# Performance work log

Hardware: AMD Instinct MI355X
Metric: run time of the kernel (lower is better)

## Reference

```python
import jax, jax.numpy as jnp
import numpy as np

B, S, H, I, NH, E = 16, 512, 1024, 4096, 16, 8
DH = H // NH
EPS = 1e-12


def layer_norm(x, g, b):
    mu = jnp.mean(x, axis=-1, keepdims=True)
    var = jnp.mean(jnp.square(x - mu), axis=-1, keepdims=True)
    return (x - mu) * jax.lax.rsqrt(var + EPS) * g + b


def setup_inputs() -> dict:
    key = jax.random.key(0)
    ks = jax.random.split(key, 16)
    s_h = 1.0 / np.sqrt(H)
    s_i = 1.0 / np.sqrt(I)
    return {
        "hidden_states": jax.random.normal(ks[0], (B, S, H), jnp.float32),
        "Wq": jax.random.normal(ks[1], (H, H), jnp.float32) * s_h,
        "bq": jnp.zeros((H,), jnp.float32),
        "Wk": jax.random.normal(ks[2], (H, H), jnp.float32) * s_h,
        "bk": jnp.zeros((H,), jnp.float32),
        "Wv": jax.random.normal(ks[3], (H, H), jnp.float32) * s_h,
        "bv": jnp.zeros((H,), jnp.float32),
        "Wo": jax.random.normal(ks[4], (H, H), jnp.float32) * s_h,
        "bo": jnp.zeros((H,), jnp.float32),
        "ln1_g": jnp.ones((H,), jnp.float32),
        "ln1_b": jnp.zeros((H,), jnp.float32),
        "ln2_g": jnp.ones((H,), jnp.float32),
        "ln2_b": jnp.zeros((H,), jnp.float32),
        "gate_W": jax.random.normal(ks[5], (H, E), jnp.float32) * s_h,
        "W_up": jax.random.normal(ks[6], (E, H, I), jnp.float32) * s_h,
        "b_up": jnp.zeros((E, I), jnp.float32),
        "W_down": jax.random.normal(ks[7], (E, I, H), jnp.float32) * s_i,
        "b_down": jnp.zeros((E, H), jnp.float32),
    }


def reference(hidden_states, Wq, bq, Wk, bk, Wv, bv, Wo, bo,
              ln1_g, ln1_b, ln2_g, ln2_b, gate_W, W_up, b_up, W_down, b_down):
    x = hidden_states
    # --- BERT self-attention ---
    q = (x @ Wq + bq).reshape(B, S, NH, DH)
    k = (x @ Wk + bk).reshape(B, S, NH, DH)
    v = (x @ Wv + bv).reshape(B, S, NH, DH)
    scores = jnp.einsum("bqhd,bkhd->bhqk", q, k) / np.sqrt(DH)
    probs = jax.nn.softmax(scores, axis=-1)
    ctx = jnp.einsum("bhqk,bkhd->bqhd", probs, v).reshape(B, S, H)
    # BertSelfOutput: dense + residual + LayerNorm
    attn_out = layer_norm(ctx @ Wo + bo + x, ln1_g, ln1_b)

    # --- feed_forward_chunk: pre-LN, MoE, residual (residual on attn_out) ---
    x_ln = layer_norm(attn_out, ln2_g, ln2_b)
    router_output = jnp.einsum("bsh,he->bse", x_ln, gate_W)
    router_logits = jnp.mean(router_output, axis=1)          # [B, E]
    choice = jnp.argmax(router_logits, axis=-1)              # softmax-argmax == logits-argmax

    # per-sample top-1 expert: gather each sample's expert weights, batched GEMM
    Wu = W_up[choice]                                        # [B, H, I]
    Wd = W_down[choice]                                      # [B, I, H]
    h = jax.nn.gelu(jnp.einsum("bsh,bhi->bsi", x_ln, Wu) + b_up[choice][:, None, :],
                    approximate=False)
    moe = jnp.einsum("bsi,bih->bsh", h, Wd) + b_down[choice][:, None, :]
    layer_output = moe + attn_out
    return (layer_output, router_logits)
```

## Files before the change

### kernel.cpp

```cpp
#include <hip/hip_runtime.h>


typedef __attribute__((ext_vector_type(4))) float f32x4;
typedef __attribute__((ext_vector_type(8))) short s8v;
typedef __attribute__((ext_vector_type(4))) short s4v;
typedef unsigned short u16;

#define DEV static __device__ __forceinline__

DEV u16 f2bf(float f){
  union { float f; unsigned u; } v; v.f = f;
  unsigned r = v.u + 0x7fffu + ((v.u >> 16) & 1u);
  return (u16)(r >> 16);
}

DEV f32x4 mfma16(s8v a, s8v b, f32x4 c){
  return __builtin_amdgcn_mfma_f32_16x16x32_bf16(a, b, c, 0, 0, 0);
}

DEV float wave_sum(float s){
#pragma unroll
  for (int o = 1; o < 64; o <<= 1) s += __shfl_xor(s, o);
  return s;
}

#define ASYNC_COPY16(g, l) \
  __builtin_amdgcn_global_load_lds((const __attribute__((address_space(1))) void*)(g), \
                                   (__attribute__((address_space(3))) void*)(l), 16, 0, 0)

__global__ __launch_bounds__(256) void cvt_bf16(const float* __restrict__ in,
                                                u16* __restrict__ out)
{
  const size_t i = ((size_t)blockIdx.x * 256 + threadIdx.x) * 8;
  f32x4 a = *(const f32x4*)&in[i];
  f32x4 b = *(const f32x4*)&in[i + 4];
  s8v o;
#pragma unroll
  for (int j = 0; j < 4; ++j){ o[j] = (short)f2bf(a[j]); o[4 + j] = (short)f2bf(b[j]); }
  *(s8v*)&out[i] = o;
}

__global__ __launch_bounds__(256) void transpose_w(const float* __restrict__ in,
                                                   u16* __restrict__ out, int R, int C)
{
  __shared__ float t[64][65];
  const size_t bs = (size_t)blockIdx.z * R * (size_t)C;
  in += bs; out += bs;
  const int c0 = blockIdx.x * 64, r0 = blockIdx.y * 64;
  const int tx = threadIdx.x & 63, ty = threadIdx.x >> 6;
#pragma unroll
  for (int j = 0; j < 64; j += 4) t[ty + j][tx] = in[(size_t)(r0 + ty + j) * C + c0 + tx];
  __syncthreads();
#pragma unroll
  for (int j = 0; j < 64; j += 4) out[(size_t)(c0 + ty + j) * R + r0 + tx] = f2bf(t[tx][ty + j]);
}

template<int MODE, bool SWZ>
__global__ __launch_bounds__(256, 2) void gemm_bt(
    const u16* __restrict__ A, const u16* __restrict__ Bt,
    const float* __restrict__ bias, void* __restrict__ outp,
    const float* __restrict__ resid, int M, int N, int K,
    const int* __restrict__ choice,
    long aBatch, long outBatch, long residBatch, long btExpert, long biasExpert,
    void* __restrict__ out2, void* __restrict__ out3)
{
  int bx, by, bz;
  if (SWZ){
    const int nx = gridDim.x, ny = gridDim.y;
    const int nwg = nx * ny * gridDim.z;
    int id = blockIdx.x + nx * (blockIdx.y + ny * blockIdx.z);
    if ((nwg & 7) == 0){ const int q = nwg >> 3; id = (id & 7) * q + (id >> 3); }
    bx = id % nx; const int r2 = id / nx; by = r2 % ny; bz = r2 / ny;
  } else {
    bx = blockIdx.x; by = blockIdx.y; bz = blockIdx.z;
  }
  const int z = bz;
  if (choice){
    const int e = choice[z];
    Bt   += (size_t)e * btExpert;
    bias += (size_t)e * biasExpert;
  }
  A += (size_t)z * aBatch;

  const int tid = threadIdx.x;
  const int lane = tid & 63, wid = tid >> 6;
  const int hi = lane >> 4, l15 = lane & 15;
  const int wr = wid >> 1, wc = wid & 1;
  const long row0 = (long)bx * 128;
  const long col0 = (long)by * 128;

  __shared__ __align__(16) u16 lA[2][128 * 32];
  __shared__ __align__(16) u16 lB[2][128 * 32];

  f32x4 acc[4][4];
#pragma unroll
  for (int i = 0; i < 4; ++i)
#pragma unroll
    for (int j = 0; j < 4; ++j) acc[i][j] = f32x4{0.f, 0.f, 0.f, 0.f};

  const int c1 = tid, c2 = tid + 256;
  const u16* sA1 = A  + (row0 + (c1 >> 2)) * (size_t)K + (c1 & 3) * 8;
  const u16* sA2 = A  + (row0 + (c2 >> 2)) * (size_t)K + (c2 & 3) * 8;
  const u16* sB1 = Bt + (col0 + (c1 >> 2)) * (size_t)K + (c1 & 3) * 8;
  const u16* sB2 = Bt + (col0 + (c2 >> 2)) * (size_t)K + (c2 & 3) * 8;

#define GSTAGE(bsel) do { \
  ASYNC_COPY16(sA1, &lA[bsel][c1 * 8]); \
  ASYNC_COPY16(sA2, &lA[bsel][c2 * 8]); \
  ASYNC_COPY16(sB1, &lB[bsel][c1 * 8]); \
  ASYNC_COPY16(sB2, &lB[bsel][c2 * 8]); \
  sA1 += 32; sA2 += 32; sB1 += 32; sB2 += 32; \
} while (0)

  const int nk = K >> 5;
  GSTAGE(0);
  __syncthreads();

  for (int t = 0; t < nk; ++t){
    const int cur = t & 1;
    if (t + 1 < nk) GSTAGE(cur ^ 1);
    s8v af[4], bfr[4];
#pragma unroll
    for (int mi = 0; mi < 4; ++mi)
      af[mi] = *(const s8v*)&lA[cur][(wr * 64 + mi * 16 + l15) * 32 + hi * 8];
#pragma unroll
    for (int ni = 0; ni < 4; ++ni)
      bfr[ni] = *(const s8v*)&lB[cur][(wc * 64 + ni * 16 + l15) * 32 + hi * 8];
#pragma unroll
    for (int mi = 0; mi < 4; ++mi)
#pragma unroll
      for (int ni = 0; ni < 4; ++ni)
        acc[mi][ni] = mfma16(af[mi], bfr[ni], acc[mi][ni]);
    __syncthreads();
  }
#undef GSTAGE

#pragma unroll
  for (int mi = 0; mi < 4; ++mi){
    const long rowb = row0 + wr * 64 + mi * 16 + hi * 4;
#pragma unroll
    for (int ni = 0; ni < 4; ++ni){
      const long col = col0 + wc * 64 + ni * 16 + l15;
      const float bv = bias[col];
#pragma unroll
      for (int r = 0; r < 4; ++r){
        const long row = rowb + r;
        float v = acc[mi][ni][r] + bv;
        if (MODE == 2){
          float* o = (float*)outp + (size_t)z * outBatch;
          const float* rs = resid + (size_t)z * residBatch;
          o[row * N + col] = v + rs[row * N + col];
        } else if (MODE == 0){
          u16* o = (u16*)outp + (size_t)z * outBatch;
          o[row * N + col] = f2bf(v);
        } else if (MODE == 1){
          u16* o = (u16*)outp + (size_t)z * outBatch;
          const float gv = 0.5f * v * (1.0f + erff(v * 0.70710678118654752f));
          o[row * N + col] = f2bf(gv);
        } else if (MODE == 3){
          const int bb = (int)(row >> 9), ss = (int)(row & 511);
          const int hh = (int)(col >> 6), dd = (int)(col & 63);
          ((u16*)outp)[(((size_t)(bb * 16 + hh)) * 64 + dd) * 512 + ss] = f2bf(v);
        } else {
          const int seg = (int)(col >> 10), lc = (int)(col & 1023);
          const u16 bv16 = f2bf(v);
          if (seg == 0)      ((u16*)outp)[row * 1024 + lc] = bv16;
          else if (seg == 1) ((u16*)out2)[row * 1024 + lc] = bv16;
          else {
            const int bb = (int)(row >> 9), ss = (int)(row & 511);
            const int hh = lc >> 6, dd = lc & 63;
            ((u16*)out3)[(((size_t)(bb * 16 + hh)) * 64 + dd) * 512 + ss] = bv16;
          }
        }
      }
    }
  }
}

__global__ __launch_bounds__(256) void attn_fwd(
    const u16* __restrict__ qb, const u16* __restrict__ kb,
    const u16* __restrict__ vt, u16* __restrict__ ctx)
{
  const int tid = threadIdx.x;
  const int lane = tid & 63, wid = tid >> 6;
  const int hi = lane >> 4, l15 = lane & 15;
  const int h = blockIdx.y, b = blockIdx.z;
  const int q0 = blockIdx.x * 128 + wid * 32;

  const u16* kp0 = kb + (size_t)b * 512 * 1024 + h * 64;
  const u16* vp0 = vt + ((size_t)(b * 16 + h)) * 64 * 512;

  __shared__ __align__(16) u16 lK[2][64 * 64];
  __shared__ __align__(16) u16 lV[2][64 * 64];
  __shared__ __align__(16) u16 lP[4][2][16][72];

#define STAGE(bsel, k0s) do { \
  _Pragma("unroll") \
  for (int i = 0; i < 2; ++i){ \
    const int idx = i * 256 + tid; \
    const int row = idx >> 3, seg = idx & 7; \
    const int sc = ((seg ^ (row & 7)) << 3); \
    ASYNC_COPY16(kp0 + (size_t)((k0s) + row) * 1024 + sc, &lK[bsel][idx * 8]); \
    ASYNC_COPY16(vp0 + (size_t)row * 512 + (k0s) + sc,    &lV[bsel][idx * 8]); \
  } \
} while (0)

  const u16* qp = qb + ((size_t)b * 512 + q0) * 1024 + h * 64;
  s8v qf[2][2];
#pragma unroll
  for (int qt = 0; qt < 2; ++qt)
#pragma unroll
    for (int st = 0; st < 2; ++st)
      qf[qt][st] = *(const s8v*)&qp[(size_t)(qt * 16 + l15) * 1024 + st * 32 + hi * 8];

  f32x4 o[2][4];
#pragma unroll
  for (int qt = 0; qt < 2; ++qt)
#pragma unroll
    for (int mi = 0; mi < 4; ++mi) o[qt][mi] = f32x4{0.f, 0.f, 0.f, 0.f};
  float mrun[2] = {-3e38f, -3e38f}, lrun[2] = {0.f, 0.f};

  STAGE(0, 0);
  __syncthreads();

  for (int t = 0; t < 8; ++t){
    const int buf = t & 1;
    if (t < 7) STAGE(buf ^ 1, (t + 1) * 64);

    f32x4 s[2][4];
#pragma unroll
    for (int qt = 0; qt < 2; ++qt)
#pragma unroll
      for (int kt = 0; kt < 4; ++kt) s[qt][kt] = f32x4{0.f, 0.f, 0.f, 0.f};
#pragma unroll
    for (int st = 0; st < 2; ++st){
      s8v kf[4];
#pragma unroll
      for (int kt = 0; kt < 4; ++kt){
        const int row = kt * 16 + l15;
        kf[kt] = *(const s8v*)&lK[buf][row * 64 + (((st * 4 + hi) ^ (row & 7)) << 3)];
      }
#pragma unroll
      for (int qt = 0; qt < 2; ++qt)
#pragma unroll
        for (int kt = 0; kt < 4; ++kt)
          s[qt][kt] = mfma16(kf[kt], qf[qt][st], s[qt][kt]);
    }

#pragma unroll
    for (int qt = 0; qt < 2; ++qt){
      float mx = s[qt][0][0];
#pragma unroll
      for (int kt = 0; kt < 4; ++kt)
#pragma unroll
        for (int r = 0; r < 4; ++r) mx = fmaxf(mx, s[qt][kt][r]);
      mx *= 0.125f;
      mx = fmaxf(mx, __shfl_xor(mx, 16));
      mx = fmaxf(mx, __shfl_xor(mx, 32));
      const float mnew = fmaxf(mrun[qt], mx);
      const float alpha = __expf(mrun[qt] - mnew);
      mrun[qt] = mnew;
      float ps = 0.f;
#pragma unroll
      for (int kt = 0; kt < 4; ++kt){
        s4v pk;
#pragma unroll
        for (int r = 0; r < 4; ++r){
          const float p = __expf(s[qt][kt][r] * 0.125f - mnew);
          ps += p; pk[r] = (short)f2bf(p);
        }
        *(s4v*)&lP[wid][qt][l15][kt * 16 + 4 * hi] = pk;
      }
      ps += __shfl_xor(ps, 16);
      ps += __shfl_xor(ps, 32);
      lrun[qt] = lrun[qt] * alpha + ps;
#pragma unroll
      for (int mi = 0; mi < 4; ++mi)
#pragma unroll
        for (int r = 0; r < 4; ++r) o[qt][mi][r] *= alpha;
    }

#pragma unroll
    for (int ks = 0; ks < 2; ++ks){
      s8v vf[4];
#pragma unroll
      for (int mi = 0; mi < 4; ++mi){
        const int row = mi * 16 + l15;
        vf[mi] = *(const s8v*)&lV[buf][row * 64 + (((ks * 4 + hi) ^ (row & 7)) << 3)];
      }
#pragma unroll
      for (int qt = 0; qt < 2; ++qt){
        const s8v pf = *(const s8v*)&lP[wid][qt][l15][ks * 32 + 8 * hi];
#pragma unroll
        for (int mi = 0; mi < 4; ++mi)
          o[qt][mi] = mfma16(vf[mi], pf, o[qt][mi]);
      }
    }
    __syncthreads();
  }
#undef STAGE

#pragma unroll
  for (int qt = 0; qt < 2; ++qt){
    const float inv = 1.f / lrun[qt];
    u16* cp = ctx + ((size_t)b * 512 + q0 + qt * 16 + l15) * 1024 + h * 64;
#pragma unroll
    for (int mi = 0; mi < 4; ++mi)
#pragma unroll
      for (int r = 0; r < 4; ++r)
        cp[mi * 16 + 4 * hi + r] = f2bf(o[qt][mi][r] * inv);
  }
}

__global__ __launch_bounds__(256, 2) void ln12_colsum(
    float* __restrict__ t, const float* __restrict__ g1, const float* __restrict__ b1,
    const float* __restrict__ g2, const float* __restrict__ b2,
    u16* __restrict__ xln, float* __restrict__ colsum)
{
  const int b = blockIdx.y;
  const int wid = threadIdx.x >> 6, lane = threadIdx.x & 63;
  __shared__ float cacc[1024];
  for (int i = threadIdx.x; i < 1024; i += 256) cacc[i] = 0.f;
  __syncthreads();
  float acc[16];
#pragma unroll
  for (int i = 0; i < 16; ++i) acc[i] = 0.f;
  const int rbase = b * 512 + blockIdx.x * 64 + wid * 16;
  for (int rr = 0; rr < 16; ++rr){
    float* p = t + (size_t)(rbase + rr) * 1024;
    f32x4 v[4];
#pragma unroll
    for (int c = 0; c < 4; ++c) v[c] = *(const f32x4*)&p[c * 256 + lane * 4];
    float s = 0.f;
#pragma unroll
    for (int c = 0; c < 4; ++c) s += v[c][0] + v[c][1] + v[c][2] + v[c][3];
    const float mu = wave_sum(s) * (1.f / 1024.f);
    float s2 = 0.f;
#pragma unroll
    for (int c = 0; c < 4; ++c)
#pragma unroll
      for (int j = 0; j < 4; ++j){ const float d = v[c][j] - mu; s2 += d * d; }
    const float rs = rsqrtf(wave_sum(s2) * (1.f / 1024.f) + 1e-12f);
    float y1s = 0.f;
#pragma unroll
    for (int c = 0; c < 4; ++c){
      const f32x4 gg = *(const f32x4*)&g1[c * 256 + lane * 4];
      const f32x4 bb = *(const f32x4*)&b1[c * 256 + lane * 4];
#pragma unroll
      for (int j = 0; j < 4; ++j){
        v[c][j] = (v[c][j] - mu) * rs * gg[j] + bb[j];
        y1s += v[c][j];
      }
      *(f32x4*)&p[c * 256 + lane * 4] = v[c];
    }
    const float mu2 = wave_sum(y1s) * (1.f / 1024.f);
    float s22 = 0.f;
#pragma unroll
    for (int c = 0; c < 4; ++c)
#pragma unroll
      for (int j = 0; j < 4; ++j){ const float d = v[c][j] - mu2; s22 += d * d; }
    const float rs2 = rsqrtf(wave_sum(s22) * (1.f / 1024.f) + 1e-12f);
    u16* op = xln + (size_t)(rbase + rr) * 1024;
#pragma unroll
    for (int c = 0; c < 4; ++c){
      const f32x4 gg = *(const f32x4*)&g2[c * 256 + lane * 4];
      const f32x4 bb = *(const f32x4*)&b2[c * 256 + lane * 4];
      s4v ov;
#pragma unroll
      for (int j = 0; j < 4; ++j){
        const float y = (v[c][j] - mu2) * rs2 * gg[j] + bb[j];
        acc[c * 4 + j] += y;
        ov[j] = (short)f2bf(y);
      }
      *(s4v*)&op[c * 256 + lane * 4] = ov;
    }
  }
#pragma unroll
  for (int c = 0; c < 4; ++c)
#pragma unroll
    for (int j = 0; j < 4; ++j)
      atomicAdd(&cacc[c * 256 + lane * 4 + j], acc[c * 4 + j]);
  __syncthreads();
  for (int i = threadIdx.x; i < 1024; i += 256) atomicAdd(&colsum[b * 1024 + i], cacc[i]);
}

__global__ void router_argmax(const float* __restrict__ colsum, const float* __restrict__ gate,
                              float* __restrict__ logits, int* __restrict__ choice)
{
  const int b = blockIdx.x, lane = threadIdx.x;
  float pa[8];
#pragma unroll
  for (int e = 0; e < 8; ++e) pa[e] = 0.f;
  for (int it = 0; it < 16; ++it){
    const int hh = it * 64 + lane;
    const float c = colsum[b * 1024 + hh];
    const float* gp = gate + (size_t)hh * 8;
#pragma unroll
    for (int e = 0; e < 8; ++e) pa[e] += c * gp[e];
  }
#pragma unroll
  for (int e = 0; e < 8; ++e) pa[e] = wave_sum(pa[e]);
  if (lane == 0){
    float best = -3e38f; int bi = 0;
#pragma unroll
    for (int e = 0; e < 8; ++e){
      const float lg = pa[e] * (1.f / 512.f);
      logits[b * 8 + e] = lg;
      if (lg > best){ best = lg; bi = e; }
    }
    choice[b] = bi;
  }
}

extern "C" void kernel_launch(void* const* d_in, const int* in_sizes, int n_in,
                              void* d_out, int out_size, void* d_ws, size_t ws_size,
                              hipStream_t stream)
{
  const float* x    = (const float*)d_in[0];
  const float* Wq   = (const float*)d_in[1];
  const float* bq   = (const float*)d_in[2];
  const float* Wk   = (const float*)d_in[3];
  const float* bk   = (const float*)d_in[4];
  const float* Wv   = (const float*)d_in[5];
  const float* bv   = (const float*)d_in[6];
  const float* Wo   = (const float*)d_in[7];
  const float* bo   = (const float*)d_in[8];
  const float* ln1g = (const float*)d_in[9];
  const float* ln1b = (const float*)d_in[10];
  const float* ln2g = (const float*)d_in[11];
  const float* ln2b = (const float*)d_in[12];
  const float* gate = (const float*)d_in[13];
  const float* Wup  = (const float*)d_in[14];
  const float* bup  = (const float*)d_in[15];
  const float* Wdn  = (const float*)d_in[16];
  const float* bdn  = (const float*)d_in[17];

  size_t off = 0;
  char* wsb = (char*)d_ws;
  auto take = [&](size_t n) -> void* {
    void* p = wsb + off; off += (n + 255) & ~(size_t)255; return p;
  };
  u16*   x_bf  = (u16*)take(8192ull * 1024 * 2);
  u16*   Wqt   = (u16*)take(1024ull * 1024 * 2);
  u16*   Wkt   = (u16*)take(1024ull * 1024 * 2);
  u16*   Wvt   = (u16*)take(1024ull * 1024 * 2);
  u16*   Wot   = (u16*)take(1024ull * 1024 * 2);
  u16*   q_bf  = (u16*)take(8192ull * 1024 * 2);
  u16*   k_bf  = (u16*)take(8192ull * 1024 * 2);
  u16*   vt_bf = (u16*)take(8192ull * 1024 * 2);
  float* tmp   = (float*)take(8192ull * 1024 * 4);
  u16*   Wupt  = (u16*)take(8ull * 4096 * 1024 * 2);
  u16*   Wdnt  = (u16*)take(8ull * 1024 * 4096 * 2);
  u16*   h_bf  = (u16*)take(8192ull * 4096 * 2);
  float* colsum = (float*)take(16ull * 1024 * 4);
  int*   choice = (int*)take(256);
  float* qkvb  = (float*)take(3072 * 4);

  u16* ctx = x_bf;
  u16* xln = q_bf;
  float* logits = (float*)d_out + 8388608;

  cvt_bf16<<<4096, 256, 0, stream>>>(x, x_bf);
  transpose_w<<<dim3(16, 16, 1), 256, 0, stream>>>(Wq,  Wqt,  1024, 1024);
  transpose_w<<<dim3(16, 16, 1), 256, 0, stream>>>(Wk,  Wkt,  1024, 1024);
  transpose_w<<<dim3(16, 16, 1), 256, 0, stream>>>(Wv,  Wvt,  1024, 1024);
  transpose_w<<<dim3(16, 16, 1), 256, 0, stream>>>(Wo,  Wot,  1024, 1024);
  transpose_w<<<dim3(64, 16, 8), 256, 0, stream>>>(Wup, Wupt, 1024, 4096);
  transpose_w<<<dim3(16, 64, 8), 256, 0, stream>>>(Wdn, Wdnt, 4096, 1024);
  hipMemcpyAsync(qkvb,        bq, 1024 * 4, hipMemcpyDeviceToDevice, stream);
  hipMemcpyAsync(qkvb + 1024, bk, 1024 * 4, hipMemcpyDeviceToDevice, stream);
  hipMemcpyAsync(qkvb + 2048, bv, 1024 * 4, hipMemcpyDeviceToDevice, stream);

  gemm_bt<4, false><<<dim3(64, 24, 1), 256, 0, stream>>>(x_bf, Wqt, qkvb, q_bf,
      nullptr, 8192, 3072, 1024, nullptr, 0, 0, 0, 0, 0, k_bf, vt_bf);

  attn_fwd<<<dim3(4, 16, 16), 256, 0, stream>>>(q_bf, k_bf, vt_bf, ctx);

  gemm_bt<2, false><<<dim3(64, 8, 1), 256, 0, stream>>>(ctx, Wot, bo, tmp, x,
      8192, 1024, 1024, nullptr, 0, 0, 0, 0, 0, nullptr, nullptr);
  hipMemsetAsync(colsum, 0, 16 * 1024 * sizeof(float), stream);
  ln12_colsum<<<dim3(8, 16), 256, 0, stream>>>(tmp, ln1g, ln1b, ln2g, ln2b, xln, colsum);
  router_argmax<<<16, 64, 0, stream>>>(colsum, gate, logits, choice);

  gemm_bt<1, true><<<dim3(4, 32, 16), 256, 0, stream>>>(xln, Wupt, bup, h_bf, nullptr,
      512, 4096, 1024, choice, 512ll * 1024, 512ll * 4096, 0, 4096ll * 1024, 4096,
      nullptr, nullptr);
  gemm_bt<2, true><<<dim3(4, 8, 16), 256, 0, stream>>>(h_bf, Wdnt, bdn, d_out, tmp,
      512, 1024, 4096, choice, 512ll * 4096, 512ll * 1024, 512ll * 1024, 1024ll * 4096, 1024,
      nullptr, nullptr);
}
```

Baseline: 535.0 us.

## Deepen GEMM LDS pipeline to four stages and XOR-swizzle shared tiles

The bf16 MFMA GEMM now keeps three async global-to-LDS loads in flight across four LDS slots, using explicit vmcnt waits instead of a double buffer with a trailing barrier. The LDS layout is also XOR-swizzled per row so that fragment reads spread across banks. This targets global-load latency exposure and LDS bank conflicts in the GEMMs, at the cost of doubling LDS per block, which may lower occupancy. It also relies on the async-copy instruction count matching the hand-written vmcnt values.

New measurement: 610.4 us. 1.14x slower.

```diff
diff --git a/kernel.cpp b/kernel.cpp
--- a/kernel.cpp
+++ b/kernel.cpp
@@ -89,8 +89,8 @@
   const long row0 = (long)bx * 128;
   const long col0 = (long)by * 128;
 
-  __shared__ __align__(16) u16 lA[2][128 * 32];
-  __shared__ __align__(16) u16 lB[2][128 * 32];
+  __shared__ __align__(16) u16 lA[4][128 * 32];
+  __shared__ __align__(16) u16 lB[4][128 * 32];
 
   f32x4 acc[4][4];
 #pragma unroll
@@ -99,39 +99,49 @@
     for (int j = 0; j < 4; ++j) acc[i][j] = f32x4{0.f, 0.f, 0.f, 0.f};
 
   const int c1 = tid, c2 = tid + 256;
-  const u16* sA1 = A  + (row0 + (c1 >> 2)) * (size_t)K + (c1 & 3) * 8;
-  const u16* sA2 = A  + (row0 + (c2 >> 2)) * (size_t)K + (c2 & 3) * 8;
-  const u16* sB1 = Bt + (col0 + (c1 >> 2)) * (size_t)K + (c1 & 3) * 8;
-  const u16* sB2 = Bt + (col0 + (c2 >> 2)) * (size_t)K + (c2 & 3) * 8;
-
-#define GSTAGE(bsel) do { \
-  ASYNC_COPY16(sA1, &lA[bsel][c1 * 8]); \
-  ASYNC_COPY16(sA2, &lA[bsel][c2 * 8]); \
-  ASYNC_COPY16(sB1, &lB[bsel][c1 * 8]); \
-  ASYNC_COPY16(sB2, &lB[bsel][c2 * 8]); \
+  const int r1 = c1 >> 2, r2 = c2 >> 2;
+  const int s1 = ((c1 & 3) ^ (r1 & 3)) * 8, s2 = ((c2 & 3) ^ (r2 & 3)) * 8;
+  const u16* sA1 = A  + (row0 + r1) * (size_t)K + s1;
+  const u16* sA2 = A  + (row0 + r2) * (size_t)K + s2;
+  const u16* sB1 = Bt + (col0 + r1) * (size_t)K + s1;
+  const u16* sB2 = Bt + (col0 + r2) * (size_t)K + s2;
+
+#define GSTAGE(slot) do { \
+  ASYNC_COPY16(sA1, &lA[slot][c1 * 8]); \
+  ASYNC_COPY16(sA2, &lA[slot][c2 * 8]); \
+  ASYNC_COPY16(sB1, &lB[slot][c1 * 8]); \
+  ASYNC_COPY16(sB2, &lB[slot][c2 * 8]); \
   sA1 += 32; sA2 += 32; sB1 += 32; sB2 += 32; \
 } while (0)
 
   const int nk = K >> 5;
-  GSTAGE(0);
-  __syncthreads();
+  GSTAGE(0); GSTAGE(1); GSTAGE(2);
 
   for (int t = 0; t < nk; ++t){
-    const int cur = t & 1;
-    if (t + 1 < nk) GSTAGE(cur ^ 1);
+    const int ahead = nk - 1 - t;
+    if (ahead >= 2)      asm volatile("s_waitcnt vmcnt(8)" ::: "memory");
+    else if (ahead == 1) asm volatile("s_waitcnt vmcnt(4)" ::: "memory");
+    else                 asm volatile("s_waitcnt vmcnt(0)" ::: "memory");
+    __syncthreads();
+    if (t + 3 < nk) GSTAGE((t + 3) & 3);
+
+    const int cur = t & 3;
     s8v af[4], bfr[4];
 #pragma unroll
-    for (int mi = 0; mi < 4; ++mi)
-      af[mi] = *(const s8v*)&lA[cur][(wr * 64 + mi * 16 + l15) * 32 + hi * 8];
-#pragma unroll
-    for (int ni = 0; ni < 4; ++ni)
-      bfr[ni] = *(const s8v*)&lB[cur][(wc * 64 + ni * 16 + l15) * 32 + hi * 8];
+    for (int mi = 0; mi < 4; ++mi){
+      const int R = wr * 64 + mi * 16 + l15;
+      af[mi] = *(const s8v*)&lA[cur][R * 32 + ((hi ^ (R & 3)) << 3)];
+    }
+#pragma unroll
+    for (int ni = 0; ni < 4; ++ni){
+      const int C = wc * 64 + ni * 16 + l15;
+      bfr[ni] = *(const s8v*)&lB[cur][C * 32 + ((hi ^ (C & 3)) << 3)];
+    }
 #pragma unroll
     for (int mi = 0; mi < 4; ++mi)
 #pragma unroll
       for (int ni = 0; ni < 4; ++ni)
         acc[mi][ni] = mfma16(af[mi], bfr[ni], acc[mi][ni]);
-    __syncthreads();
   }
 #undef GSTAGE
 
```

## Enlarge GEMM tile to 256x128 with triple-buffered LDS and XOR swizzle

Applied to the files above, without the earlier changes.

The bf16 GEMM tile grows from 128x128 to 256x128, so each wave now computes 8x4 MFMA blocks, and grids shrink to match. Shared memory becomes a 3-stage ring with explicit vmcnt waits and raw barriers in place of the double buffer with __syncthreads. An XOR swizzle on the LDS column is added to avoid bank conflicts, and setprio is raised around the MFMA burst. The second template flag is also turned on for the dense GEMMs, which may enable the workgroup remap. The intent is better operand reuse and deeper load/compute overlap, at the cost of more registers and LDS, lower occupancy, and fewer workgroups for the small MoE GEMMs.

New measurement: 602.5 us. 12.6% more time.

```diff
diff --git a/kernel.cpp b/kernel.cpp
--- a/kernel.cpp
+++ b/kernel.cpp
@@ -86,58 +86,76 @@
   const int lane = tid & 63, wid = tid >> 6;
   const int hi = lane >> 4, l15 = lane & 15;
   const int wr = wid >> 1, wc = wid & 1;
-  const long row0 = (long)bx * 128;
+  const long row0 = (long)bx * 256;
   const long col0 = (long)by * 128;
 
-  __shared__ __align__(16) u16 lA[2][128 * 32];
-  __shared__ __align__(16) u16 lB[2][128 * 32];
-
-  f32x4 acc[4][4];
-#pragma unroll
-  for (int i = 0; i < 4; ++i)
+  __shared__ __align__(16) u16 lA[3][256 * 32];
+  __shared__ __align__(16) u16 lB[3][128 * 32];
+
+  f32x4 acc[8][4];
+#pragma unroll
+  for (int i = 0; i < 8; ++i)
 #pragma unroll
     for (int j = 0; j < 4; ++j) acc[i][j] = f32x4{0.f, 0.f, 0.f, 0.f};
 
-  const int c1 = tid, c2 = tid + 256;
-  const u16* sA1 = A  + (row0 + (c1 >> 2)) * (size_t)K + (c1 & 3) * 8;
-  const u16* sA2 = A  + (row0 + (c2 >> 2)) * (size_t)K + (c2 & 3) * 8;
-  const u16* sB1 = Bt + (col0 + (c1 >> 2)) * (size_t)K + (c1 & 3) * 8;
-  const u16* sB2 = Bt + (col0 + (c2 >> 2)) * (size_t)K + (c2 & 3) * 8;
-
-#define GSTAGE(bsel) do { \
-  ASYNC_COPY16(sA1, &lA[bsel][c1 * 8]); \
-  ASYNC_COPY16(sA2, &lA[bsel][c2 * 8]); \
-  ASYNC_COPY16(sB1, &lB[bsel][c1 * 8]); \
-  ASYNC_COPY16(sB2, &lB[bsel][c2 * 8]); \
-  sA1 += 32; sA2 += 32; sB1 += 32; sB2 += 32; \
+  const int srow = tid >> 2;
+  const int scol = (((tid & 3) ^ (srow & 3)) << 3);
+  const u16* pA[4]; const u16* pB[2];
+#pragma unroll
+  for (int j = 0; j < 4; ++j) pA[j] = A  + (row0 + j * 64 + srow) * (size_t)K + scol;
+#pragma unroll
+  for (int j = 0; j < 2; ++j) pB[j] = Bt + (col0 + j * 64 + srow) * (size_t)K + scol;
+
+#define GSTAGE(S_) do { \
+  _Pragma("unroll") \
+  for (int j = 0; j < 4; ++j) ASYNC_COPY16(pA[j], &lA[S_][(j * 256 + tid) * 8]); \
+  _Pragma("unroll") \
+  for (int j = 0; j < 2; ++j) ASYNC_COPY16(pB[j], &lB[S_][(j * 256 + tid) * 8]); \
+  _Pragma("unroll") \
+  for (int j = 0; j < 4; ++j) pA[j] += 32; \
+  _Pragma("unroll") \
+  for (int j = 0; j < 2; ++j) pB[j] += 32; \
 } while (0)
 
+  const int baseA = (wr * 128 + l15) * 32 + ((hi ^ (l15 & 3)) << 3);
+  const int baseB = (wc * 64  + l15) * 32 + ((hi ^ (l15 & 3)) << 3);
+
+#define ITER(S_, S2_, WSTR_, DOSTAGE_) do { \
+  asm volatile("s_waitcnt vmcnt(" WSTR_ ")" ::: "memory"); \
+  __builtin_amdgcn_s_barrier(); \
+  __builtin_amdgcn_sched_barrier(0); \
+  asm volatile("" ::: "memory"); \
+  if (DOSTAGE_) GSTAGE(S2_); \
+  s8v af[8], bfv[4]; \
+  _Pragma("unroll") \
+  for (int mi = 0; mi < 8; ++mi) af[mi] = *(const s8v*)&lA[S_][baseA + mi * 512]; \
+  _Pragma("unroll") \
+  for (int ni = 0; ni < 4; ++ni) bfv[ni] = *(const s8v*)&lB[S_][baseB + ni * 512]; \
+  __builtin_amdgcn_s_setprio(1); \
+  _Pragma("unroll") \
+  for (int mi = 0; mi < 8; ++mi) \
+    _Pragma("unroll") \
+    for (int ni = 0; ni < 4; ++ni) \
+      acc[mi][ni] = mfma16(af[mi], bfv[ni], acc[mi][ni]); \
+  __builtin_amdgcn_s_setprio(0); \
+} while (0)
+
   const int nk = K >> 5;
-  GSTAGE(0);
-  __syncthreads();
-
-  for (int t = 0; t < nk; ++t){
-    const int cur = t & 1;
-    if (t + 1 < nk) GSTAGE(cur ^ 1);
-    s8v af[4], bfr[4];
-#pragma unroll
-    for (int mi = 0; mi < 4; ++mi)
-      af[mi] = *(const s8v*)&lA[cur][(wr * 64 + mi * 16 + l15) * 32 + hi * 8];
-#pragma unroll
-    for (int ni = 0; ni < 4; ++ni)
-      bfr[ni] = *(const s8v*)&lB[cur][(wc * 64 + ni * 16 + l15) * 32 + hi * 8];
-#pragma unroll
-    for (int mi = 0; mi < 4; ++mi)
-#pragma unroll
-      for (int ni = 0; ni < 4; ++ni)
-        acc[mi][ni] = mfma16(af[mi], bfr[ni], acc[mi][ni]);
-    __syncthreads();
-  }
+  GSTAGE(0); GSTAGE(1);
+
+  for (int t = 0; t < nk - 2; t += 3){
+    ITER(0, 2, "6", 1);
+    ITER(1, 0, "6", 1);
+    ITER(2, 1, "6", 1);
+  }
+  ITER(0, 0, "6", 0);
+  ITER(1, 0, "0", 0);
+#undef ITER
 #undef GSTAGE
 
 #pragma unroll
-  for (int mi = 0; mi < 4; ++mi){
-    const long rowb = row0 + wr * 64 + mi * 16 + hi * 4;
+  for (int mi = 0; mi < 8; ++mi){
+    const long rowb = row0 + wr * 128 + mi * 16 + hi * 4;
 #pragma unroll
     for (int ni = 0; ni < 4; ++ni){
       const long col = col0 + wc * 64 + ni * 16 + l15;
@@ -150,18 +168,11 @@
           float* o = (float*)outp + (size_t)z * outBatch;
           const float* rs = resid + (size_t)z * residBatch;
           o[row * N + col] = v + rs[row * N + col];
-        } else if (MODE == 0){
-          u16* o = (u16*)outp + (size_t)z * outBatch;
-          o[row * N + col] = f2bf(v);
         } else if (MODE == 1){
           u16* o = (u16*)outp + (size_t)z * outBatch;
           const float gv = 0.5f * v * (1.0f + erff(v * 0.70710678118654752f));
           o[row * N + col] = f2bf(gv);
-        } else if (MODE == 3){
-          const int bb = (int)(row >> 9), ss = (int)(row & 511);
-          const int hh = (int)(col >> 6), dd = (int)(col & 63);
-          ((u16*)outp)[(((size_t)(bb * 16 + hh)) * 64 + dd) * 512 + ss] = f2bf(v);
-        } else {
+        } else if (MODE == 4){
           const int seg = (int)(col >> 10), lc = (int)(col & 1023);
           const u16 bv16 = f2bf(v);
           if (seg == 0)      ((u16*)outp)[row * 1024 + lc] = bv16;
@@ -471,21 +482,21 @@
   hipMemcpyAsync(qkvb + 1024, bk, 1024 * 4, hipMemcpyDeviceToDevice, stream);
   hipMemcpyAsync(qkvb + 2048, bv, 1024 * 4, hipMemcpyDeviceToDevice, stream);
 
-  gemm_bt<4, false><<<dim3(64, 24, 1), 256, 0, stream>>>(x_bf, Wqt, qkvb, q_bf,
+  gemm_bt<4, true><<<dim3(32, 24, 1), 256, 0, stream>>>(x_bf, Wqt, qkvb, q_bf,
       nullptr, 8192, 3072, 1024, nullptr, 0, 0, 0, 0, 0, k_bf, vt_bf);
 
   attn_fwd<<<dim3(4, 16, 16), 256, 0, stream>>>(q_bf, k_bf, vt_bf, ctx);
 
-  gemm_bt<2, false><<<dim3(64, 8, 1), 256, 0, stream>>>(ctx, Wot, bo, tmp, x,
+  gemm_bt<2, true><<<dim3(32, 8, 1), 256, 0, stream>>>(ctx, Wot, bo, tmp, x,
       8192, 1024, 1024, nullptr, 0, 0, 0, 0, 0, nullptr, nullptr);
   hipMemsetAsync(colsum, 0, 16 * 1024 * sizeof(float), stream);
   ln12_colsum<<<dim3(8, 16), 256, 0, stream>>>(tmp, ln1g, ln1b, ln2g, ln2b, xln, colsum);
   router_argmax<<<16, 64, 0, stream>>>(colsum, gate, logits, choice);
 
-  gemm_bt<1, true><<<dim3(4, 32, 16), 256, 0, stream>>>(xln, Wupt, bup, h_bf, nullptr,
+  gemm_bt<1, true><<<dim3(2, 32, 16), 256, 0, stream>>>(xln, Wupt, bup, h_bf, nullptr,
       512, 4096, 1024, choice, 512ll * 1024, 512ll * 4096, 0, 4096ll * 1024, 4096,
       nullptr, nullptr);
-  gemm_bt<2, true><<<dim3(4, 8, 16), 256, 0, stream>>>(h_bf, Wdnt, bdn, d_out, tmp,
+  gemm_bt<2, true><<<dim3(2, 8, 16), 256, 0, stream>>>(h_bf, Wdnt, bdn, d_out, tmp,
       512, 1024, 4096, choice, 512ll * 4096, 512ll * 1024, 512ll * 1024, 1024ll * 4096, 1024,
       nullptr, nullptr);
 }
```
